# Optimization experiments

Measured on AMD Instinct MI355X. Metric: run time of the kernel, lower is better.

The kernel has to match this reference:

```python
import jax, jax.numpy as jnp
import numpy as np

BN_EPS = 1e-5

def setup_inputs() -> dict:
    key = jax.random.key(0)
    ks = jax.random.split(key, 8)
    N, E, D = 50000, 800000, 128
    x = jax.random.normal(ks[0], (N, D), dtype=jnp.float32)
    edge_index = jax.random.randint(ks[1], (2, E), 0, N, dtype=jnp.int64)
    s = 1.0 / np.sqrt(D)
    W1 = jax.random.uniform(ks[2], (D, D), jnp.float32, -s, s)
    b1 = jax.random.uniform(ks[3], (D,), jnp.float32, -s, s)
    W2 = jax.random.uniform(ks[4], (D, D), jnp.float32, -s, s)
    b2 = jax.random.uniform(ks[5], (D,), jnp.float32, -s, s)
    g1 = jnp.ones((D,), jnp.float32); be1 = jnp.zeros((D,), jnp.float32)
    g2 = jnp.ones((D,), jnp.float32); be2 = jnp.zeros((D,), jnp.float32)
    eps = jnp.zeros((), jnp.float32)  # learnable GIN epsilon (train_eps=True)
    return {"x": x, "edge_index": edge_index, "eps": eps,
            "W1": W1, "b1": b1, "g1": g1, "be1": be1,
            "W2": W2, "b2": b2, "g2": g2, "be2": be2}

def _batchnorm(h, gamma, beta):
    # training-mode BatchNorm1d over node axis (biased variance)
    mu = jnp.mean(h, axis=0)
    var = jnp.mean(jnp.square(h - mu), axis=0)
    return (h - mu) * jax.lax.rsqrt(var + BN_EPS) * gamma + beta

def reference(x, edge_index, eps, W1, b1, g1, be1, W2, b2, g2, be2):
    N = x.shape[0]
    src, dst = edge_index[0], edge_index[1]
    # GIN aggregation: sum of neighbor features (scatter-add to target nodes)
    agg = jax.ops.segment_sum(x[src], dst, num_segments=N)  # [N, D]
    h = (1.0 + eps) * x + agg
    # MLP: Linear -> BN -> ReLU -> Linear
    h = h @ W1.T + b1
    h = jax.nn.relu(_batchnorm(h, g1, be1))
    h = h @ W2.T + b2
    # outer BatchNorm + ReLU
    return jax.nn.relu(_batchnorm(h, g2, be2))
```

## Files before the change

kernel.cpp:

```cpp
#include <hip/hip_runtime.h>
#include <hip/hip_bf16.h>


#define DIM 128
#define KMAX 64

typedef unsigned short u16;
typedef __attribute__((ext_vector_type(8))) short short8;
typedef __attribute__((ext_vector_type(4))) float f32x4;

__device__ inline u16 f2b(float f) {
  unsigned int u = __builtin_bit_cast(unsigned int, f);
  u += 0x7fffu + ((u >> 16) & 1u);
  return (u16)(u >> 16);
}

__global__ __launch_bounds__(256) void prep_kernel(
    const float* __restrict__ W1, const float* __restrict__ W2,
    int* __restrict__ cursor, u16* __restrict__ wb1, u16* __restrict__ wb2) {
  int i = blockIdx.x * blockDim.x + threadIdx.x;
  const int stride = gridDim.x * blockDim.x;
  for (; i < 20948; i += stride) {
    if (i < 12756) {
      int4 z = {0, 0, 0, 0};
      reinterpret_cast<int4*>(cursor)[i] = z;
    } else if (i < 16852) {
      const int j = i - 12756;
      const float4 v = reinterpret_cast<const float4*>(W1)[j];
      ushort4 o = {f2b(v.x), f2b(v.y), f2b(v.z), f2b(v.w)};
      reinterpret_cast<ushort4*>(wb1)[j] = o;
    } else {
      const int j = i - 16852;
      const float4 v = reinterpret_cast<const float4*>(W2)[j];
      ushort4 o = {f2b(v.x), f2b(v.y), f2b(v.z), f2b(v.w)};
      reinterpret_cast<ushort4*>(wb2)[j] = o;
    }
  }
}

__global__ __launch_bounds__(256) void reorder_kernel(
    const int* __restrict__ ei, int* __restrict__ cursor,
    u16* __restrict__ buckets, int E) {
  const int t = blockIdx.x * blockDim.x + threadIdx.x;
  const int stride = gridDim.x * blockDim.x;
  for (int e = t; e < E; e += 2 * stride) {
    const int e2 = e + stride;
    const int s1 = ei[e], d1 = ei[E + e];
    const bool v2 = e2 < E;
    int s2 = 0, d2 = 0;
    if (v2) { s2 = ei[e2]; d2 = ei[E + e2]; }
    const int p1 = atomicAdd(&cursor[d1], 1);
    const int p2 = v2 ? atomicAdd(&cursor[d2], 1) : 0;
    if (p1 < KMAX) buckets[d1 * KMAX + p1] = (u16)s1;
    if (v2 && p2 < KMAX) buckets[d2 * KMAX + p2] = (u16)s2;
  }
}

__global__ __launch_bounds__(256) void aggregate_kernel(
    const float* __restrict__ x, const int* __restrict__ cursor,
    const u16* __restrict__ buckets, const float* __restrict__ epsp,
    u16* __restrict__ hb, int N) {
  const int g = threadIdx.x >> 5;
  const int lane = threadIdx.x & 31;
  const int node = blockIdx.x * 8 + g;
  if (node >= N) return;
  const float k = 1.0f + epsp[0];
  int d = cursor[node];
  if (d > KMAX) d = KMAX;
  const u16* bk = buckets + node * KMAX;

  const float4 xv = *reinterpret_cast<const float4*>(x + (long long)node * DIM + lane * 4);
  float ax = k * xv.x, ay = k * xv.y, az = k * xv.z, aw = k * xv.w;

  int j = 0;
  for (; j + 4 <= d; j += 4) {
    const int s0 = bk[j], s1 = bk[j + 1], s2 = bk[j + 2], s3 = bk[j + 3];
    const float4 v0 = *reinterpret_cast<const float4*>(x + (long long)s0 * DIM + lane * 4);
    const float4 v1 = *reinterpret_cast<const float4*>(x + (long long)s1 * DIM + lane * 4);
    const float4 v2 = *reinterpret_cast<const float4*>(x + (long long)s2 * DIM + lane * 4);
    const float4 v3 = *reinterpret_cast<const float4*>(x + (long long)s3 * DIM + lane * 4);
    ax += v0.x + v1.x + v2.x + v3.x;
    ay += v0.y + v1.y + v2.y + v3.y;
    az += v0.z + v1.z + v2.z + v3.z;
    aw += v0.w + v1.w + v2.w + v3.w;
  }
  for (; j < d; ++j) {
    const int s = bk[j];
    const float4 v = *reinterpret_cast<const float4*>(x + (long long)s * DIM + lane * 4);
    ax += v.x; ay += v.y; az += v.z; aw += v.w;
  }
  ushort4 o = {f2b(ax), f2b(ay), f2b(az), f2b(aw)};
  *reinterpret_cast<ushort4*>(hb + (long long)node * DIM + lane * 4) = o;
}

template <int FUSE>
__global__ __launch_bounds__(256) void gemm_mfma_kernel(
    const void* __restrict__ Av, const u16* __restrict__ Wb,
    const float* __restrict__ bias, const float* __restrict__ ss,
    float* __restrict__ C, int N) {
  const int lane = threadIdx.x & 63;
  const int wid = threadIdx.x >> 6;
  const int l15 = lane & 15;
  const int lg = lane >> 4;
  const int wrow = blockIdx.x * 64 + wid * 16;

  f32x4 acc[8];
#pragma unroll
  for (int ni = 0; ni < 8; ++ni) acc[ni] = (f32x4){0.f, 0.f, 0.f, 0.f};

  int arow = wrow + l15;
  if (arow >= N) arow = N - 1;

#pragma unroll
  for (int kb = 0; kb < 4; ++kb) {
    const int k0 = kb * 32 + lg * 8;
    short8 a;
    if (FUSE) {
      const float* A = (const float*)Av + (long long)arow * DIM + k0;
      const float4 v0 = *reinterpret_cast<const float4*>(A);
      const float4 v1 = *reinterpret_cast<const float4*>(A + 4);
      const float4 sc0 = *reinterpret_cast<const float4*>(ss + k0);
      const float4 sc1 = *reinterpret_cast<const float4*>(ss + k0 + 4);
      const float4 sh0 = *reinterpret_cast<const float4*>(ss + DIM + k0);
      const float4 sh1 = *reinterpret_cast<const float4*>(ss + DIM + k0 + 4);
      a[0] = (short)f2b(fmaxf(fmaf(v0.x, sc0.x, sh0.x), 0.f));
      a[1] = (short)f2b(fmaxf(fmaf(v0.y, sc0.y, sh0.y), 0.f));
      a[2] = (short)f2b(fmaxf(fmaf(v0.z, sc0.z, sh0.z), 0.f));
      a[3] = (short)f2b(fmaxf(fmaf(v0.w, sc0.w, sh0.w), 0.f));
      a[4] = (short)f2b(fmaxf(fmaf(v1.x, sc1.x, sh1.x), 0.f));
      a[5] = (short)f2b(fmaxf(fmaf(v1.y, sc1.y, sh1.y), 0.f));
      a[6] = (short)f2b(fmaxf(fmaf(v1.z, sc1.z, sh1.z), 0.f));
      a[7] = (short)f2b(fmaxf(fmaf(v1.w, sc1.w, sh1.w), 0.f));
    } else {
      a = *reinterpret_cast<const short8*>((const u16*)Av + (long long)arow * DIM + k0);
    }
#pragma unroll
    for (int ni = 0; ni < 8; ++ni) {
      const short8 b = *reinterpret_cast<const short8*>(Wb + (ni * 16 + l15) * DIM + k0);
      acc[ni] = __builtin_amdgcn_mfma_f32_16x16x32_bf16(a, b, acc[ni], 0, 0, 0);
    }
  }

#pragma unroll
  for (int ni = 0; ni < 8; ++ni) {
    const int col = ni * 16 + l15;
    const float bv = bias[col];
    const int rbase = wrow + lg * 4;
#pragma unroll
    for (int r = 0; r < 4; ++r) {
      const int row = rbase + r;
      if (row < N) C[(long long)row * DIM + col] = acc[ni][r] + bv;
    }
  }
}

__global__ __launch_bounds__(256) void stats_kernel(
    const float* __restrict__ H, float* __restrict__ stats, int N) {
  __shared__ float red[256];
  const int col = threadIdx.x & 127;
  const int sub = threadIdx.x >> 7;
  float s = 0.f, sq = 0.f;
  for (int row = blockIdx.x * 2 + sub; row < N; row += gridDim.x * 2) {
    const float v = H[(long long)row * DIM + col];
    s += v;
    sq = fmaf(v, v, sq);
  }
  red[threadIdx.x] = s;
  __syncthreads();
  if (sub == 0) unsafeAtomicAdd(&stats[col], s + red[threadIdx.x + 128]);
  __syncthreads();
  red[threadIdx.x] = sq;
  __syncthreads();
  if (sub == 0) unsafeAtomicAdd(&stats[DIM + col], sq + red[threadIdx.x + 128]);
}

__global__ void finalize_kernel(const float* __restrict__ stats,
                                const float* __restrict__ gamma,
                                const float* __restrict__ beta,
                                float* __restrict__ ss, float Ninv) {
  const int j = threadIdx.x;
  const float mu = stats[j] * Ninv;
  const float var = stats[DIM + j] * Ninv - mu * mu;
  const float sc = gamma[j] * rsqrtf(var + 1e-5f);
  ss[j] = sc;
  ss[DIM + j] = beta[j] - mu * sc;
}

__global__ __launch_bounds__(256) void bnrelu_kernel(
    float* __restrict__ out, const float* __restrict__ ss, int total4) {
  float4* __restrict__ o4 = reinterpret_cast<float4*>(out);
  int i = blockIdx.x * blockDim.x + threadIdx.x;
  const int stride = gridDim.x * blockDim.x;
  for (; i < total4; i += stride) {
    const int c0 = (i * 4) & (DIM - 1);
    float4 v = o4[i];
    v.x = fmaxf(fmaf(v.x, ss[c0 + 0], ss[DIM + c0 + 0]), 0.f);
    v.y = fmaxf(fmaf(v.y, ss[c0 + 1], ss[DIM + c0 + 1]), 0.f);
    v.z = fmaxf(fmaf(v.z, ss[c0 + 2], ss[DIM + c0 + 2]), 0.f);
    v.w = fmaxf(fmaf(v.w, ss[c0 + 3], ss[DIM + c0 + 3]), 0.f);
    o4[i] = v;
  }
}

extern "C" void kernel_launch(void* const* d_in, const int* in_sizes, int n_in,
                              void* d_out, int out_size, void* d_ws, size_t ws_size,
                              hipStream_t stream) {
  const float* x   = (const float*)d_in[0];
  const int*   ei  = (const int*)d_in[1];
  const float* eps = (const float*)d_in[2];
  const float* W1  = (const float*)d_in[3];
  const float* b1  = (const float*)d_in[4];
  const float* g1  = (const float*)d_in[5];
  const float* be1 = (const float*)d_in[6];
  const float* W2  = (const float*)d_in[7];
  const float* b2  = (const float*)d_in[8];
  const float* g2  = (const float*)d_in[9];
  const float* be2 = (const float*)d_in[10];
  float* out = (float*)d_out;

  const int N = in_sizes[0] / DIM;
  const int E = in_sizes[1] / 2;

  u16* hb      = (u16*)d_ws;
  u16* wb1     = hb + (size_t)N * DIM;
  u16* wb2     = wb1 + DIM * DIM;
  u16* buckets = wb2 + DIM * DIM;
  int* cursor  = (int*)(buckets + (size_t)N * KMAX);
  float* stats1 = (float*)(cursor + N);
  float* ss1    = stats1 + 256;
  float* stats2 = ss1 + 256;
  float* ss2    = stats2 + 256;

  prep_kernel<<<82, 256, 0, stream>>>(W1, W2, cursor, wb1, wb2);
  reorder_kernel<<<2048, 256, 0, stream>>>(ei, cursor, buckets, E);
  aggregate_kernel<<<(N + 7) / 8, 256, 0, stream>>>(x, cursor, buckets, eps, hb, N);

  const int gblocks = (N + 63) / 64;
  gemm_mfma_kernel<0><<<gblocks, 256, 0, stream>>>(hb, wb1, b1, nullptr, out, N);
  stats_kernel<<<512, 256, 0, stream>>>(out, stats1, N);
  finalize_kernel<<<1, DIM, 0, stream>>>(stats1, g1, be1, ss1, 1.0f / N);
  gemm_mfma_kernel<1><<<gblocks, 256, 0, stream>>>(out, wb2, b2, ss1, out, N);
  stats_kernel<<<512, 256, 0, stream>>>(out, stats2, N);
  finalize_kernel<<<1, DIM, 0, stream>>>(stats2, g2, be2, ss2, 1.0f / N);
  bnrelu_kernel<<<2048, 256, 0, stream>>>(out, ss2, N * (DIM / 4));
}
```

Measured before the change: 304.4 us.

## Fuse BN stats into GEMM epilogue, gather bf16 features, split edge cursors

Converts x to bf16 in the prep kernel so the neighbor gather reads half the bytes. Splits each node's bucket cursor into two ways to reduce atomic contention in the reorder step. Computes the batchnorm sum and sum-of-squares inside the GEMM epilogue via shuffles and shared memory, which removes both standalone stats kernels and their extra passes over the activations. The cost is extra rounding of x to bf16 and a per-way cap of 32 neighbors per node.

Measured after the change: 274.0 us. 10.0% less time.

```diff
diff --git a/kernel.cpp b/kernel.cpp
--- a/kernel.cpp
+++ b/kernel.cpp
@@ -3,6 +3,8 @@
 
 
 #define DIM 128
+#define SUB 2
+#define CAP 32
 #define KMAX 64
 
 typedef unsigned short u16;
@@ -14,26 +16,38 @@
   u += 0x7fffu + ((u >> 16) & 1u);
   return (u16)(u >> 16);
 }
+__device__ inline float b2f(u16 b) {
+  unsigned int u = ((unsigned int)b) << 16;
+  return __builtin_bit_cast(float, u);
+}
 
 __global__ __launch_bounds__(256) void prep_kernel(
     const float* __restrict__ W1, const float* __restrict__ W2,
-    int* __restrict__ cursor, u16* __restrict__ wb1, u16* __restrict__ wb2) {
+    const float* __restrict__ x, int* __restrict__ cursor,
+    u16* __restrict__ wb1, u16* __restrict__ wb2, u16* __restrict__ xb,
+    int Z, int NX) {
   int i = blockIdx.x * blockDim.x + threadIdx.x;
   const int stride = gridDim.x * blockDim.x;
-  for (; i < 20948; i += stride) {
-    if (i < 12756) {
+  const int e1 = Z + 4096, e2 = Z + 8192, e3 = Z + 8192 + NX;
+  for (; i < e3; i += stride) {
+    if (i < Z) {
       int4 z = {0, 0, 0, 0};
       reinterpret_cast<int4*>(cursor)[i] = z;
-    } else if (i < 16852) {
-      const int j = i - 12756;
+    } else if (i < e1) {
+      const int j = i - Z;
       const float4 v = reinterpret_cast<const float4*>(W1)[j];
       ushort4 o = {f2b(v.x), f2b(v.y), f2b(v.z), f2b(v.w)};
       reinterpret_cast<ushort4*>(wb1)[j] = o;
-    } else {
-      const int j = i - 16852;
+    } else if (i < e2) {
+      const int j = i - e1;
       const float4 v = reinterpret_cast<const float4*>(W2)[j];
       ushort4 o = {f2b(v.x), f2b(v.y), f2b(v.z), f2b(v.w)};
       reinterpret_cast<ushort4*>(wb2)[j] = o;
+    } else {
+      const int j = i - e2;
+      const float4 v = reinterpret_cast<const float4*>(x)[j];
+      ushort4 o = {f2b(v.x), f2b(v.y), f2b(v.z), f2b(v.w)};
+      reinterpret_cast<ushort4*>(xb)[j] = o;
     }
   }
 }
@@ -43,21 +57,22 @@
     u16* __restrict__ buckets, int E) {
   const int t = blockIdx.x * blockDim.x + threadIdx.x;
   const int stride = gridDim.x * blockDim.x;
+  const int way = t & 1;
   for (int e = t; e < E; e += 2 * stride) {
     const int e2 = e + stride;
     const int s1 = ei[e], d1 = ei[E + e];
     const bool v2 = e2 < E;
     int s2 = 0, d2 = 0;
     if (v2) { s2 = ei[e2]; d2 = ei[E + e2]; }
-    const int p1 = atomicAdd(&cursor[d1], 1);
-    const int p2 = v2 ? atomicAdd(&cursor[d2], 1) : 0;
-    if (p1 < KMAX) buckets[d1 * KMAX + p1] = (u16)s1;
-    if (v2 && p2 < KMAX) buckets[d2 * KMAX + p2] = (u16)s2;
+    const int p1 = atomicAdd(&cursor[d1 * SUB + way], 1);
+    const int p2 = v2 ? atomicAdd(&cursor[d2 * SUB + way], 1) : 0;
+    if (p1 < CAP) buckets[d1 * KMAX + way * CAP + p1] = (u16)s1;
+    if (v2 && p2 < CAP) buckets[d2 * KMAX + way * CAP + p2] = (u16)s2;
   }
 }
 
 __global__ __launch_bounds__(256) void aggregate_kernel(
-    const float* __restrict__ x, const int* __restrict__ cursor,
+    const u16* __restrict__ xb, const int* __restrict__ cursor,
     const u16* __restrict__ buckets, const float* __restrict__ epsp,
     u16* __restrict__ hb, int N) {
   const int g = threadIdx.x >> 5;
@@ -65,29 +80,34 @@
   const int node = blockIdx.x * 8 + g;
   if (node >= N) return;
   const float k = 1.0f + epsp[0];
-  int d = cursor[node];
-  if (d > KMAX) d = KMAX;
+  int c0 = cursor[node * SUB + 0]; if (c0 > CAP) c0 = CAP;
+  int c1 = cursor[node * SUB + 1]; if (c1 > CAP) c1 = CAP;
   const u16* bk = buckets + node * KMAX;
 
-  const float4 xv = *reinterpret_cast<const float4*>(x + (long long)node * DIM + lane * 4);
-  float ax = k * xv.x, ay = k * xv.y, az = k * xv.z, aw = k * xv.w;
-
-  int j = 0;
-  for (; j + 4 <= d; j += 4) {
-    const int s0 = bk[j], s1 = bk[j + 1], s2 = bk[j + 2], s3 = bk[j + 3];
-    const float4 v0 = *reinterpret_cast<const float4*>(x + (long long)s0 * DIM + lane * 4);
-    const float4 v1 = *reinterpret_cast<const float4*>(x + (long long)s1 * DIM + lane * 4);
-    const float4 v2 = *reinterpret_cast<const float4*>(x + (long long)s2 * DIM + lane * 4);
-    const float4 v3 = *reinterpret_cast<const float4*>(x + (long long)s3 * DIM + lane * 4);
-    ax += v0.x + v1.x + v2.x + v3.x;
-    ay += v0.y + v1.y + v2.y + v3.y;
-    az += v0.z + v1.z + v2.z + v3.z;
-    aw += v0.w + v1.w + v2.w + v3.w;
-  }
-  for (; j < d; ++j) {
-    const int s = bk[j];
-    const float4 v = *reinterpret_cast<const float4*>(x + (long long)s * DIM + lane * 4);
-    ax += v.x; ay += v.y; az += v.z; aw += v.w;
+  const ushort4 xv = *reinterpret_cast<const ushort4*>(xb + (long long)node * DIM + lane * 4);
+  float ax = k * b2f(xv.x), ay = k * b2f(xv.y), az = k * b2f(xv.z), aw = k * b2f(xv.w);
+
+#pragma unroll
+  for (int w = 0; w < SUB; ++w) {
+    const int d = w ? c1 : c0;
+    const u16* b = bk + w * CAP;
+    int j = 0;
+    for (; j + 4 <= d; j += 4) {
+      const int s0 = b[j], s1 = b[j + 1], s2 = b[j + 2], s3 = b[j + 3];
+      const ushort4 v0 = *reinterpret_cast<const ushort4*>(xb + (long long)s0 * DIM + lane * 4);
+      const ushort4 v1 = *reinterpret_cast<const ushort4*>(xb + (long long)s1 * DIM + lane * 4);
+      const ushort4 v2 = *reinterpret_cast<const ushort4*>(xb + (long long)s2 * DIM + lane * 4);
+      const ushort4 v3 = *reinterpret_cast<const ushort4*>(xb + (long long)s3 * DIM + lane * 4);
+      ax += b2f(v0.x) + b2f(v1.x) + b2f(v2.x) + b2f(v3.x);
+      ay += b2f(v0.y) + b2f(v1.y) + b2f(v2.y) + b2f(v3.y);
+      az += b2f(v0.z) + b2f(v1.z) + b2f(v2.z) + b2f(v3.z);
+      aw += b2f(v0.w) + b2f(v1.w) + b2f(v2.w) + b2f(v3.w);
+    }
+    for (; j < d; ++j) {
+      const int s = b[j];
+      const ushort4 v = *reinterpret_cast<const ushort4*>(xb + (long long)s * DIM + lane * 4);
+      ax += b2f(v.x); ay += b2f(v.y); az += b2f(v.z); aw += b2f(v.w);
+    }
   }
   ushort4 o = {f2b(ax), f2b(ay), f2b(az), f2b(aw)};
   *reinterpret_cast<ushort4*>(hb + (long long)node * DIM + lane * 4) = o;
@@ -97,7 +117,9 @@
 __global__ __launch_bounds__(256) void gemm_mfma_kernel(
     const void* __restrict__ Av, const u16* __restrict__ Wb,
     const float* __restrict__ bias, const float* __restrict__ ss,
-    float* __restrict__ C, int N) {
+    float* __restrict__ C, float* __restrict__ stats, int N) {
+  __shared__ float sred[4][DIM];
+  __shared__ float qred[4][DIM];
   const int lane = threadIdx.x & 63;
   const int wid = threadIdx.x >> 6;
   const int l15 = lane & 15;
@@ -141,37 +163,34 @@
     }
   }
 
+  const int rbase = wrow + lg * 4;
 #pragma unroll
   for (int ni = 0; ni < 8; ++ni) {
     const int col = ni * 16 + l15;
     const float bv = bias[col];
-    const int rbase = wrow + lg * 4;
+    float s = 0.f, q = 0.f;
 #pragma unroll
     for (int r = 0; r < 4; ++r) {
       const int row = rbase + r;
-      if (row < N) C[(long long)row * DIM + col] = acc[ni][r] + bv;
-    }
-  }
-}
-
-__global__ __launch_bounds__(256) void stats_kernel(
-    const float* __restrict__ H, float* __restrict__ stats, int N) {
-  __shared__ float red[256];
-  const int col = threadIdx.x & 127;
-  const int sub = threadIdx.x >> 7;
-  float s = 0.f, sq = 0.f;
-  for (int row = blockIdx.x * 2 + sub; row < N; row += gridDim.x * 2) {
-    const float v = H[(long long)row * DIM + col];
-    s += v;
-    sq = fmaf(v, v, sq);
-  }
-  red[threadIdx.x] = s;
+      if (row < N) {
+        const float v = acc[ni][r] + bv;
+        C[(long long)row * DIM + col] = v;
+        s += v;
+        q = fmaf(v, v, q);
+      }
+    }
+    s += __shfl_xor(s, 16); s += __shfl_xor(s, 32);
+    q += __shfl_xor(q, 16); q += __shfl_xor(q, 32);
+    if (lg == 0) { sred[wid][col] = s; qred[wid][col] = q; }
+  }
   __syncthreads();
-  if (sub == 0) unsafeAtomicAdd(&stats[col], s + red[threadIdx.x + 128]);
-  __syncthreads();
-  red[threadIdx.x] = sq;
-  __syncthreads();
-  if (sub == 0) unsafeAtomicAdd(&stats[DIM + col], sq + red[threadIdx.x + 128]);
+  const int t = threadIdx.x;
+  if (t < DIM) {
+    unsafeAtomicAdd(&stats[t], sred[0][t] + sred[1][t] + sred[2][t] + sred[3][t]);
+  } else {
+    const int c = t - DIM;
+    unsafeAtomicAdd(&stats[DIM + c], qred[0][c] + qred[1][c] + qred[2][c] + qred[3][c]);
+  }
 }
 
 __global__ void finalize_kernel(const float* __restrict__ stats,
@@ -226,21 +245,24 @@
   u16* wb2     = wb1 + DIM * DIM;
   u16* buckets = wb2 + DIM * DIM;
   int* cursor  = (int*)(buckets + (size_t)N * KMAX);
-  float* stats1 = (float*)(cursor + N);
+  float* stats1 = (float*)(cursor + SUB * N);
   float* ss1    = stats1 + 256;
   float* stats2 = ss1 + 256;
   float* ss2    = stats2 + 256;
 
-  prep_kernel<<<82, 256, 0, stream>>>(W1, W2, cursor, wb1, wb2);
+  u16* xb = (u16*)d_out;
+
+  const int Z  = (SUB * N + 1024 + 3) / 4;
+  const int NX = N * DIM / 4;
+
+  prep_kernel<<<2048, 256, 0, stream>>>(W1, W2, x, cursor, wb1, wb2, xb, Z, NX);
   reorder_kernel<<<2048, 256, 0, stream>>>(ei, cursor, buckets, E);
-  aggregate_kernel<<<(N + 7) / 8, 256, 0, stream>>>(x, cursor, buckets, eps, hb, N);
+  aggregate_kernel<<<(N + 7) / 8, 256, 0, stream>>>(xb, cursor, buckets, eps, hb, N);
 
   const int gblocks = (N + 63) / 64;
-  gemm_mfma_kernel<0><<<gblocks, 256, 0, stream>>>(hb, wb1, b1, nullptr, out, N);
-  stats_kernel<<<512, 256, 0, stream>>>(out, stats1, N);
+  gemm_mfma_kernel<0><<<gblocks, 256, 0, stream>>>(hb, wb1, b1, nullptr, out, stats1, N);
   finalize_kernel<<<1, DIM, 0, stream>>>(stats1, g1, be1, ss1, 1.0f / N);
-  gemm_mfma_kernel<1><<<gblocks, 256, 0, stream>>>(out, wb2, b2, ss1, out, N);
-  stats_kernel<<<512, 256, 0, stream>>>(out, stats2, N);
+  gemm_mfma_kernel<1><<<gblocks, 256, 0, stream>>>(out, wb2, b2, ss1, out, stats2, N);
   finalize_kernel<<<1, DIM, 0, stream>>>(stats2, g2, be2, ss2, 1.0f / N);
   bnrelu_kernel<<<2048, 256, 0, stream>>>(out, ss2, N * (DIM / 4));
 }
```
